# Performance work log

Measured on AMD Instinct MI355X. Metric: run time of the kernel, lower is better.

Reference implementation:

```python
import jax, jax.numpy as jnp
import numpy as np

# Log-signature at depth m=3, d channels, expressed in the full tensor basis
# (iisignature 'expanded' convention; the Lyndon-basis output of method '' is a
# fixed linear projection of these coefficients).

def _chen_step(carry, dx):
    # carry: signature levels S1 [B,d], S2 [B,d,d], S3 [B,d,d,d]
    # dx: increment of one segment, [B,d]. Segment signature E = exp(dx).
    S1, S2, S3 = carry
    E2 = 0.5 * jnp.einsum('bi,bj->bij', dx, dx)
    E3 = (1.0 / 6.0) * jnp.einsum('bi,bj,bk->bijk', dx, dx, dx)
    nS1 = S1 + dx
    nS2 = S2 + jnp.einsum('bi,bj->bij', S1, dx) + E2
    nS3 = (S3
           + jnp.einsum('bij,bk->bijk', S2, dx)
           + jnp.einsum('bi,bjk->bijk', S1, E2)
           + E3)
    return (nS1, nS2, nS3), None


def _logsig(x):
    # x: [B, L, d] path. Returns expanded log-signature [B, d + d^2 + d^3].
    B, L, d = x.shape
    dx = jnp.swapaxes(x[:, 1:] - x[:, :-1], 0, 1)  # [L-1, B, d]
    init = (jnp.zeros((B, d), x.dtype),
            jnp.zeros((B, d, d), x.dtype),
            jnp.zeros((B, d, d, d), x.dtype))
    (S1, S2, S3), _ = jax.lax.scan(_chen_step, init, dx)
    # log(1 + S) truncated at level 3 in the tensor algebra
    l1 = S1
    l2 = S2 - 0.5 * jnp.einsum('bi,bj->bij', S1, S1)
    l3 = (S3
          - 0.5 * (jnp.einsum('bi,bjk->bijk', S1, S2)
                   + jnp.einsum('bij,bk->bijk', S2, S1))
          + (1.0 / 3.0) * jnp.einsum('bi,bj,bk->bijk', S1, S1, S1))
    return jnp.concatenate(
        [l1.reshape(B, -1), l2.reshape(B, -1), l3.reshape(B, -1)], axis=-1)


def setup_inputs() -> dict:
    key = jax.random.key(0)
    B, L, d = 2048, 256, 8
    steps = 0.1 * jax.random.normal(key, (B, L, d), dtype=jnp.float32)
    x = jnp.cumsum(steps, axis=1)  # random-walk paths keep signatures well-scaled
    return {"x": x}


def reference(x):
    return _logsig(x)
```

## Files before the change

kernel.cpp:

```cpp
#include <hip/hip_runtime.h>


#define LEN 256
#define DCH 8
#define NW 4
#define CHUNK (LEN / NW)
#define OUTSTRIDE (DCH + DCH*DCH + DCH*DCH*DCH)

__global__ __launch_bounds__(256) void logsig_fused(const float* __restrict__ x,
                                                    float* __restrict__ out) {
    __shared__ __align__(16) float dxbuf[LEN][DCH];
    __shared__ __align__(16) float sig1[NW][8];
    __shared__ __align__(16) float sig2[NW][64];
    __shared__ __align__(16) float sig3[NW][512];
    __shared__ __align__(16) float s1buf[8];
    __shared__ __align__(16) float s2buf[64];

    const int tid  = threadIdx.x;
    const int w    = tid >> 6;
    const int lane = tid & 63;
    const int i    = lane >> 3;
    const int j    = lane & 7;
    const int b    = blockIdx.x;

    const float4* x4 = (const float4*)(x + (size_t)b * (LEN * DCH));
    float4* d4 = (float4*)&dxbuf[0][0];
    for (int f = tid; f < 512; f += 256) {
        float4 dv;
        if (f < 510) {
            float4 a = x4[f];
            float4 c = x4[f + 2];
            dv.x = c.x - a.x; dv.y = c.y - a.y; dv.z = c.z - a.z; dv.w = c.w - a.w;
        } else {
            dv.x = 0.f; dv.y = 0.f; dv.z = 0.f; dv.w = 0.f;
        }
        d4[f] = dv;
    }
    __syncthreads();

    float s1 = 0.f, s2 = 0.f;
    float s3[8];
#pragma unroll
    for (int k = 0; k < 8; ++k) s3[k] = 0.f;

    const float c6 = 1.f / 6.f;
    const float* base = &dxbuf[w * CHUNK][0];
    for (int tb = 0; tb < CHUNK; tb += 4) {
#pragma unroll
        for (int u = 0; u < 4; ++u) {
            const float* row = base + (tb + u) * 8;
            float4 r0 = *(const float4*)(row);
            float4 r1 = *(const float4*)(row + 4);
            float dxi = row[i];
            float dxj = row[j];
            float tt = fmaf(c6, dxi, 0.5f * s1);
            float w3 = fmaf(tt, dxj, s2);
            s3[0] = fmaf(w3, r0.x, s3[0]);
            s3[1] = fmaf(w3, r0.y, s3[1]);
            s3[2] = fmaf(w3, r0.z, s3[2]);
            s3[3] = fmaf(w3, r0.w, s3[3]);
            s3[4] = fmaf(w3, r1.x, s3[4]);
            s3[5] = fmaf(w3, r1.y, s3[5]);
            s3[6] = fmaf(w3, r1.z, s3[6]);
            s3[7] = fmaf(w3, r1.w, s3[7]);
            float uu = fmaf(0.5f, dxi, s1);
            s2 = fmaf(uu, dxj, s2);
            s1 += dxi;
        }
    }

    if (j == 0) sig1[w][i] = s1;
    sig2[w][lane] = s2;
    float* sp = &sig3[w][lane * 8];
    *(float4*)(sp)     = make_float4(s3[0], s3[1], s3[2], s3[3]);
    *(float4*)(sp + 4) = make_float4(s3[4], s3[5], s3[6], s3[7]);
    __syncthreads();

    if (w != 0) return;

    for (int c = 1; c < NW; ++c) {
        float B1i  = sig1[c][i];
        float B1j  = sig1[c][j];
        float B2ij = sig2[c][lane];
        float4 b1a = *(const float4*)&sig1[c][0];
        float4 b1b = *(const float4*)&sig1[c][4];
        const float* b2row = &sig2[c][j * 8];
        float4 b2a = *(const float4*)(b2row);
        float4 b2b = *(const float4*)(b2row + 4);
        const float* b3row = &sig3[c][lane * 8];
        float4 b3a = *(const float4*)(b3row);
        float4 b3b = *(const float4*)(b3row + 4);
        float B1k[8]  = {b1a.x, b1a.y, b1a.z, b1a.w, b1b.x, b1b.y, b1b.z, b1b.w};
        float B2jk[8] = {b2a.x, b2a.y, b2a.z, b2a.w, b2b.x, b2b.y, b2b.z, b2b.w};
        float B3[8]   = {b3a.x, b3a.y, b3a.z, b3a.w, b3b.x, b3b.y, b3b.z, b3b.w};
#pragma unroll
        for (int k = 0; k < 8; ++k)
            s3[k] = s3[k] + B3[k] + s1 * B2jk[k] + s2 * B1k[k];
        s2 = s2 + B2ij + s1 * B1j;
        s1 = s1 + B1i;
    }

    if (j == 0) s1buf[i] = s1;
    s2buf[lane] = s2;

    float S1r[8], S2rj[8];
#pragma unroll
    for (int k = 0; k < 8; ++k) S1r[k] = s1buf[k];
#pragma unroll
    for (int k = 0; k < 8; ++k) S2rj[k] = s2buf[j * 8 + k];
    float s1j = s1buf[j];

    float* ob = out + (size_t)b * OUTSTRIDE;
    if (lane < 8) ob[lane] = s1buf[lane];
    ob[8 + lane] = fmaf(-0.5f * s1, s1j, s2);

    float c3 = (1.f / 3.f) * s1 * s1j;
    float l3[8];
#pragma unroll
    for (int k = 0; k < 8; ++k)
        l3[k] = s3[k] - 0.5f * (s1 * S2rj[k] + s2 * S1r[k]) + c3 * S1r[k];
    float* p3 = ob + 72 + lane * 8;
    *(float4*)(p3)     = make_float4(l3[0], l3[1], l3[2], l3[3]);
    *(float4*)(p3 + 4) = make_float4(l3[4], l3[5], l3[6], l3[7]);
}

extern "C" void kernel_launch(void* const* d_in, const int* in_sizes, int n_in,
                              void* d_out, int out_size, void* d_ws, size_t ws_size,
                              hipStream_t stream) {
    const float* x = (const float*)d_in[0];
    float* out = (float*)d_out;
    const int B = in_sizes[0] / (LEN * DCH);
    hipLaunchKernelGGL(logsig_fused, dim3(B), dim3(256), 0, stream, x, out);
}
```

Baseline: 73.22 us.

## Transpose dx buffer in LDS and broadcast step rows via readlane

Stores the increments channel-major with padding so each lane loads eight consecutive time steps of its i and j channels with float4 reads. Each lane also loads one element, and the eight k-values per step come from wave-uniform readlane broadcasts instead of per-step LDS reads. The level-1 update is rewritten around a half-sum accumulator, which saves an operation per step. This cuts LDS traffic in the scan loop but adds scalar readlane instructions, and the transposed store may cause bank conflicts during setup.

```diff
diff --git a/kernel.cpp b/kernel.cpp
--- a/kernel.cpp
+++ b/kernel.cpp
@@ -4,12 +4,13 @@
 #define LEN 256
 #define DCH 8
 #define NW 4
-#define CHUNK (LEN / NW)
+#define CHUNK 64
+#define TPAD 260
 #define OUTSTRIDE (DCH + DCH*DCH + DCH*DCH*DCH)
 
 __global__ __launch_bounds__(256) void logsig_fused(const float* __restrict__ x,
                                                     float* __restrict__ out) {
-    __shared__ __align__(16) float dxbuf[LEN][DCH];
+    __shared__ __align__(16) float dxT[DCH][TPAD];
     __shared__ __align__(16) float sig1[NW][8];
     __shared__ __align__(16) float sig2[NW][64];
     __shared__ __align__(16) float sig3[NW][512];
@@ -24,7 +25,6 @@
     const int b    = blockIdx.x;
 
     const float4* x4 = (const float4*)(x + (size_t)b * (LEN * DCH));
-    float4* d4 = (float4*)&dxbuf[0][0];
     for (int f = tid; f < 512; f += 256) {
         float4 dv;
         if (f < 510) {
@@ -34,40 +34,70 @@
         } else {
             dv.x = 0.f; dv.y = 0.f; dv.z = 0.f; dv.w = 0.f;
         }
-        d4[f] = dv;
+        int t  = f >> 1;
+        int c0 = (f & 1) * 4;
+        dxT[c0 + 0][t] = dv.x;
+        dxT[c0 + 1][t] = dv.y;
+        dxT[c0 + 2][t] = dv.z;
+        dxT[c0 + 3][t] = dv.w;
     }
     __syncthreads();
 
-    float s1 = 0.f, s2 = 0.f;
+    float h1 = 0.f, s2 = 0.f;
     float s3[8];
 #pragma unroll
     for (int k = 0; k < 8; ++k) s3[k] = 0.f;
 
     const float c6 = 1.f / 6.f;
-    const float* base = &dxbuf[w * CHUNK][0];
-    for (int tb = 0; tb < CHUNK; tb += 4) {
-#pragma unroll
-        for (int u = 0; u < 4; ++u) {
-            const float* row = base + (tb + u) * 8;
-            float4 r0 = *(const float4*)(row);
-            float4 r1 = *(const float4*)(row + 4);
-            float dxi = row[i];
-            float dxj = row[j];
-            float tt = fmaf(c6, dxi, 0.5f * s1);
-            float w3 = fmaf(tt, dxj, s2);
-            s3[0] = fmaf(w3, r0.x, s3[0]);
-            s3[1] = fmaf(w3, r0.y, s3[1]);
-            s3[2] = fmaf(w3, r0.z, s3[2]);
-            s3[3] = fmaf(w3, r0.w, s3[3]);
-            s3[4] = fmaf(w3, r1.x, s3[4]);
-            s3[5] = fmaf(w3, r1.y, s3[5]);
-            s3[6] = fmaf(w3, r1.z, s3[6]);
-            s3[7] = fmaf(w3, r1.w, s3[7]);
-            float uu = fmaf(0.5f, dxi, s1);
-            s2 = fmaf(uu, dxj, s2);
-            s1 += dxi;
-        }
+    const float* vip = &dxT[i][w * CHUNK];
+    const float* vjp = &dxT[j][w * CHUNK];
+    const float* rvp = &dxT[lane & 7][w * CHUNK + (lane >> 3)];
+
+#define STEP(DXI, DXJ, U)                                                     \
+    do {                                                                      \
+        float dxi = (DXI), dxj = (DXJ);                                       \
+        float r0 = __int_as_float(__builtin_amdgcn_readlane(rv, 8*(U)+0));    \
+        float r1 = __int_as_float(__builtin_amdgcn_readlane(rv, 8*(U)+1));    \
+        float r2 = __int_as_float(__builtin_amdgcn_readlane(rv, 8*(U)+2));    \
+        float r3 = __int_as_float(__builtin_amdgcn_readlane(rv, 8*(U)+3));    \
+        float r4 = __int_as_float(__builtin_amdgcn_readlane(rv, 8*(U)+4));    \
+        float r5 = __int_as_float(__builtin_amdgcn_readlane(rv, 8*(U)+5));    \
+        float r6 = __int_as_float(__builtin_amdgcn_readlane(rv, 8*(U)+6));    \
+        float r7 = __int_as_float(__builtin_amdgcn_readlane(rv, 8*(U)+7));    \
+        float h1n = fmaf(0.5f, dxi, h1);                    \
+        float uu  = h1 + h1n;                              \
+        float tt  = fmaf(c6, dxi, h1);                    \
+        float w3  = fmaf(tt, dxj, s2);                                        \
+        s3[0] = fmaf(w3, r0, s3[0]);                                          \
+        s3[1] = fmaf(w3, r1, s3[1]);                                          \
+        s3[2] = fmaf(w3, r2, s3[2]);                                          \
+        s3[3] = fmaf(w3, r3, s3[3]);                                          \
+        s3[4] = fmaf(w3, r4, s3[4]);                                          \
+        s3[5] = fmaf(w3, r5, s3[5]);                                          \
+        s3[6] = fmaf(w3, r6, s3[6]);                                          \
+        s3[7] = fmaf(w3, r7, s3[7]);                                          \
+        s2 = fmaf(uu, dxj, s2);                                               \
+        h1 = h1n;                                                             \
+    } while (0)
+
+    for (int tb = 0; tb < CHUNK; tb += 8) {
+        int rv = __float_as_int(rvp[tb]);
+        float4 vi0 = *(const float4*)(vip + tb);
+        float4 vi1 = *(const float4*)(vip + tb + 4);
+        float4 vj0 = *(const float4*)(vjp + tb);
+        float4 vj1 = *(const float4*)(vjp + tb + 4);
+        STEP(vi0.x, vj0.x, 0);
+        STEP(vi0.y, vj0.y, 1);
+        STEP(vi0.z, vj0.z, 2);
+        STEP(vi0.w, vj0.w, 3);
+        STEP(vi1.x, vj1.x, 4);
+        STEP(vi1.y, vj1.y, 5);
+        STEP(vi1.z, vj1.z, 6);
+        STEP(vi1.w, vj1.w, 7);
     }
+#undef STEP
+
+    float s1 = h1 + h1;
 
     if (j == 0) sig1[w][i] = s1;
     sig2[w][lane] = s2;
```

New measurement: 77.29 us. 1.06x slower.

## Store path increments as bf16 in shared memory with transposed channel layout

Applied to the files above, without the earlier changes.

Increments are truncated to bf16 and stored twice in LDS: packed per-timestep rows for the level-3 update, and a channel-major transposed copy so each thread reads eight of its own dx_i/dx_j values with one vector load. The inner loop is unrolled by 8 and tracks half of S1 to save a multiply, and warp 0 no longer writes its partial signature to shared memory. This is meant to cut LDS traffic and footprint so more blocks can be resident (launch bounds now ask for 8). The cost is bf16 truncation of every increment, which loses precision in the signature.

```diff
diff --git a/kernel.cpp b/kernel.cpp
--- a/kernel.cpp
+++ b/kernel.cpp
@@ -4,15 +4,24 @@
 #define LEN 256
 #define DCH 8
 #define NW 4
-#define CHUNK (LEN / NW)
+#define CHUNK 64
+#define TPADB 264
 #define OUTSTRIDE (DCH + DCH*DCH + DCH*DCH*DCH)
 
-__global__ __launch_bounds__(256) void logsig_fused(const float* __restrict__ x,
-                                                    float* __restrict__ out) {
-    __shared__ __align__(16) float dxbuf[LEN][DCH];
-    __shared__ __align__(16) float sig1[NW][8];
-    __shared__ __align__(16) float sig2[NW][64];
-    __shared__ __align__(16) float sig3[NW][512];
+__device__ __forceinline__ float lo16(unsigned int u) {
+    return __uint_as_float(u << 16);
+}
+__device__ __forceinline__ float hi16(unsigned int u) {
+    return __uint_as_float(u & 0xffff0000u);
+}
+
+__global__ __launch_bounds__(256, 8) void logsig_fused(const float* __restrict__ x,
+                                                       float* __restrict__ out) {
+    __shared__ __align__(16) unsigned short dxT[DCH][TPADB];
+    __shared__ __align__(16) unsigned int   rowsB[LEN * 4];
+    __shared__ __align__(16) float sig1[NW - 1][8];
+    __shared__ __align__(16) float sig2[NW - 1][64];
+    __shared__ __align__(16) float sig3[NW - 1][512];
     __shared__ __align__(16) float s1buf[8];
     __shared__ __align__(16) float s2buf[64];
 
@@ -24,7 +33,6 @@
     const int b    = blockIdx.x;
 
     const float4* x4 = (const float4*)(x + (size_t)b * (LEN * DCH));
-    float4* d4 = (float4*)&dxbuf[0][0];
     for (int f = tid; f < 512; f += 256) {
         float4 dv;
         if (f < 510) {
@@ -34,51 +42,71 @@
         } else {
             dv.x = 0.f; dv.y = 0.f; dv.z = 0.f; dv.w = 0.f;
         }
-        d4[f] = dv;
+        const int t  = f >> 1;
+        const int c0 = (f & 1) * 4;
+        const unsigned int ux = __float_as_uint(dv.x), uy = __float_as_uint(dv.y);
+        const unsigned int uz = __float_as_uint(dv.z), uw4 = __float_as_uint(dv.w);
+        rowsB[t * 4 + (f & 1) * 2 + 0] = (ux >> 16) | (uy & 0xffff0000u);
+        rowsB[t * 4 + (f & 1) * 2 + 1] = (uz >> 16) | (uw4 & 0xffff0000u);
+        dxT[c0 + 0][t] = (unsigned short)(ux >> 16);
+        dxT[c0 + 1][t] = (unsigned short)(uy >> 16);
+        dxT[c0 + 2][t] = (unsigned short)(uz >> 16);
+        dxT[c0 + 3][t] = (unsigned short)(uw4 >> 16);
     }
     __syncthreads();
 
-    float s1 = 0.f, s2 = 0.f;
+    float h1 = 0.f, s2 = 0.f;
     float s3[8];
 #pragma unroll
     for (int k = 0; k < 8; ++k) s3[k] = 0.f;
 
     const float c6 = 1.f / 6.f;
-    const float* base = &dxbuf[w * CHUNK][0];
-    for (int tb = 0; tb < CHUNK; tb += 4) {
+    const int tb0 = w * CHUNK;
+    const unsigned short* vip = &dxT[i][tb0];
+    const unsigned short* vjp = &dxT[j][tb0];
+
+    for (int g = 0; g < 8; ++g) {
+        uint4 vi8 = *(const uint4*)(vip + g * 8);
+        uint4 vj8 = *(const uint4*)(vjp + g * 8);
+        const unsigned int* rp = &rowsB[(tb0 + g * 8) * 4];
 #pragma unroll
-        for (int u = 0; u < 4; ++u) {
-            const float* row = base + (tb + u) * 8;
-            float4 r0 = *(const float4*)(row);
-            float4 r1 = *(const float4*)(row + 4);
-            float dxi = row[i];
-            float dxj = row[j];
-            float tt = fmaf(c6, dxi, 0.5f * s1);
-            float w3 = fmaf(tt, dxj, s2);
-            s3[0] = fmaf(w3, r0.x, s3[0]);
-            s3[1] = fmaf(w3, r0.y, s3[1]);
-            s3[2] = fmaf(w3, r0.z, s3[2]);
-            s3[3] = fmaf(w3, r0.w, s3[3]);
-            s3[4] = fmaf(w3, r1.x, s3[4]);
-            s3[5] = fmaf(w3, r1.y, s3[5]);
-            s3[6] = fmaf(w3, r1.z, s3[6]);
-            s3[7] = fmaf(w3, r1.w, s3[7]);
-            float uu = fmaf(0.5f, dxi, s1);
+        for (int u = 0; u < 8; ++u) {
+            uint4 R = *(const uint4*)(rp + u * 4);
+            unsigned int dvi = ((const unsigned int*)&vi8)[u >> 1];
+            unsigned int dvj = ((const unsigned int*)&vj8)[u >> 1];
+            float dxi = (u & 1) ? hi16(dvi) : lo16(dvi);
+            float dxj = (u & 1) ? hi16(dvj) : lo16(dvj);
+            float h1n = fmaf(0.5f, dxi, h1);
+            float uu  = h1 + h1n;
+            float tt  = fmaf(c6, dxi, h1);
+            float w3  = fmaf(tt, dxj, s2);
+            s3[0] = fmaf(w3, lo16(R.x), s3[0]);
+            s3[1] = fmaf(w3, hi16(R.x), s3[1]);
+            s3[2] = fmaf(w3, lo16(R.y), s3[2]);
+            s3[3] = fmaf(w3, hi16(R.y), s3[3]);
+            s3[4] = fmaf(w3, lo16(R.z), s3[4]);
+            s3[5] = fmaf(w3, hi16(R.z), s3[5]);
+            s3[6] = fmaf(w3, lo16(R.w), s3[6]);
+            s3[7] = fmaf(w3, hi16(R.w), s3[7]);
             s2 = fmaf(uu, dxj, s2);
-            s1 += dxi;
+            h1 = h1n;
         }
     }
 
-    if (j == 0) sig1[w][i] = s1;
-    sig2[w][lane] = s2;
-    float* sp = &sig3[w][lane * 8];
-    *(float4*)(sp)     = make_float4(s3[0], s3[1], s3[2], s3[3]);
-    *(float4*)(sp + 4) = make_float4(s3[4], s3[5], s3[6], s3[7]);
+    float s1 = h1 + h1;
+
+    if (w != 0) {
+        if (j == 0) sig1[w - 1][i] = s1;
+        sig2[w - 1][lane] = s2;
+        float* sp = &sig3[w - 1][lane * 8];
+        *(float4*)(sp)     = make_float4(s3[0], s3[1], s3[2], s3[3]);
+        *(float4*)(sp + 4) = make_float4(s3[4], s3[5], s3[6], s3[7]);
+    }
     __syncthreads();
 
     if (w != 0) return;
 
-    for (int c = 1; c < NW; ++c) {
+    for (int c = 0; c < NW - 1; ++c) {
         float B1i  = sig1[c][i];
         float B1j  = sig1[c][j];
         float B2ij = sig2[c][lane];
```

Measured after the change: 163.2 us. 2.23x slower.
